# Performance work log

Measured on AMD Instinct MI355X. Metric: run time of the kernel, lower is better.

## Reference

```python
import jax, jax.numpy as jnp
import numpy as np

NEG_SLOPE = 0.01  # F.leaky_relu default


def gcn_conv(x, src, dst, norm, W, b, n_nodes):
    """PyG-style GCNConv: h = x @ W; out[i] = sum_{(j->i)} norm_e * h[j] + b.
    src/dst/norm already include self-loops and symmetric D^-1/2 A D^-1/2 weights."""
    h = x @ W                                   # [N, out]
    msgs = h[src] * norm[:, None]               # [E+N, out] gather
    out = jax.ops.segment_sum(msgs, dst, num_segments=n_nodes)  # scatter-add
    return out + b


def _build_norm(edge_idx, n_nodes):
    """Add self-loops and compute symmetric GCN normalization coefficients."""
    loops = jnp.arange(n_nodes, dtype=edge_idx.dtype)
    src = jnp.concatenate([edge_idx[0], loops])
    dst = jnp.concatenate([edge_idx[1], loops])
    deg = jax.ops.segment_sum(jnp.ones_like(dst, dtype=jnp.float32), dst,
                              num_segments=n_nodes)
    dinv = jnp.where(deg > 0, jax.lax.rsqrt(jnp.maximum(deg, 1.0)), 0.0)
    norm = dinv[src] * dinv[dst]
    return src, dst, norm


def setup_inputs() -> dict:
    key = jax.random.key(0)
    k = jax.random.split(key, 8)
    N, E, nfeat, nhid = 50000, 800000, 64, 64
    x = jax.random.normal(k[0], (N, nfeat), dtype=jnp.float32)
    edge_idx = jax.random.randint(k[1], (2, E), 0, N, dtype=jnp.int32)
    # inverted dropout mask, p=0.5 -> values in {0, 2}
    drop_mask = (jax.random.uniform(k[2], (N, nhid)) >= 0.5).astype(jnp.float32) * 2.0
    # glorot-style GCNConv weights + zero bias (PyG defaults)
    s1 = (6.0 / (nfeat + nhid)) ** 0.5
    s2 = (6.0 / (nhid + nhid // 2)) ** 0.5
    W1 = jax.random.uniform(k[3], (nfeat, nhid), minval=-s1, maxval=s1, dtype=jnp.float32)
    b1 = jnp.zeros((nhid,), dtype=jnp.float32)
    W2 = jax.random.uniform(k[4], (nhid, nhid // 2), minval=-s2, maxval=s2, dtype=jnp.float32)
    b2 = jnp.zeros((nhid // 2,), dtype=jnp.float32)
    return {"x": x, "edge_idx": edge_idx, "drop_mask": drop_mask,
            "W1": W1, "b1": b1, "W2": W2, "b2": b2}


def reference(x, edge_idx, drop_mask, W1, b1, W2, b2):
    n_nodes = x.shape[0]
    src, dst, norm = _build_norm(edge_idx, n_nodes)
    h = jax.nn.leaky_relu(gcn_conv(x, src, dst, norm, W1, b1, n_nodes), NEG_SLOPE)
    h = h * drop_mask  # F.dropout(p=0.5) with precomputed inverted mask
    out = jax.nn.leaky_relu(gcn_conv(h, src, dst, norm, W2, b2, n_nodes), NEG_SLOPE)
    return out
```

## Files before the change

kernel.cpp:

```cpp
#include <hip/hip_runtime.h>
#include <hip/hip_fp16.h>

#define NEG_SLOPE 0.01f
typedef unsigned int uint;
typedef unsigned short u16;

#define NBK 256
#define CHUNK 4096
#define KPT 16
#define GROWS 16

__device__ __forceinline__ void acc_row(uint2 v, float w,
                                        float& ax, float& ay, float& az, float& aw) {
    float2 f0 = __half22float2(*reinterpret_cast<__half2*>(&v.x));
    float2 f1 = __half22float2(*reinterpret_cast<__half2*>(&v.y));
    ax = fmaf(f0.x, w, ax); ay = fmaf(f0.y, w, ay);
    az = fmaf(f1.x, w, az); aw = fmaf(f1.y, w, aw);
}

__device__ __forceinline__ float wbits(uint rec) {
    u16 b = (u16)(rec >> 16);
    __half h;
    *reinterpret_cast<u16*>(&h) = b;
    return __half2float(h);
}

__global__ __launch_bounds__(256) void bucket_hist(const int* __restrict__ dst,
                                                   uint* __restrict__ hist,
                                                   int E) {
    __shared__ uint lh[NBK];
    int t = threadIdx.x;
    lh[t] = 0u;
    __syncthreads();
    int base = blockIdx.x * CHUNK;
#pragma unroll
    for (int r = 0; r < 4; ++r) {
        int e4 = base + r * 1024 + t * 4;
        if (e4 + 3 < E) {
            int4 d = *(const int4*)(dst + e4);
            atomicAdd(&lh[((uint)d.x) >> 8], 1u);
            atomicAdd(&lh[((uint)d.y) >> 8], 1u);
            atomicAdd(&lh[((uint)d.z) >> 8], 1u);
            atomicAdd(&lh[((uint)d.w) >> 8], 1u);
        } else {
            for (int e = e4; e < E && e < e4 + 4; ++e)
                atomicAdd(&lh[((uint)dst[e]) >> 8], 1u);
        }
    }
    __syncthreads();
    hist[(size_t)blockIdx.x * NBK + t] = lh[t];
}

__global__ __launch_bounds__(256) void scan_hist(uint* __restrict__ hist,
                                                 uint* __restrict__ buckTotal,
                                                 int nchunks) {
    __shared__ uint lds[256];
    int b = blockIdx.x;
    int t = threadIdx.x;
    uint carry = 0;
    for (int c0 = 0; c0 < nchunks; c0 += 256) {
        int c = c0 + t;
        uint v = (c < nchunks) ? hist[(size_t)c * NBK + b] : 0u;
        lds[t] = v;
        __syncthreads();
        for (int off = 1; off < 256; off <<= 1) {
            uint u = (t >= off) ? lds[t - off] : 0u;
            __syncthreads();
            lds[t] += u;
            __syncthreads();
        }
        uint incl = lds[t];
        if (c < nchunks) hist[(size_t)c * NBK + b] = carry + incl - v;
        uint tot = lds[255];
        __syncthreads();
        carry += tot;
    }
    if (t == 0) buckTotal[b] = carry;
}

__global__ __launch_bounds__(256) void scan256(const uint* __restrict__ buckTotal,
                                               uint* __restrict__ buckBase,
                                               int nbuck, int E) {
    __shared__ uint lds[256];
    int t = threadIdx.x;
    uint v = buckTotal[t];
    lds[t] = v;
    __syncthreads();
    for (int off = 1; off < 256; off <<= 1) {
        uint u = (t >= off) ? lds[t - off] : 0u;
        __syncthreads();
        lds[t] += u;
        __syncthreads();
    }
    buckBase[t] = (t < nbuck) ? (lds[t] - v) : (uint)E;
    if (t == 0) buckBase[NBK] = (uint)E;
}

__global__ __launch_bounds__(256) void partition_edges(const int* __restrict__ src,
                                                       const int* __restrict__ dst,
                                                       const uint* __restrict__ hist,
                                                       const uint* __restrict__ buckBase,
                                                       uint* __restrict__ staging,
                                                       int E) {
    __shared__ uint lh[NBK];
    __shared__ uint runbase[NBK];
    int t = threadIdx.x;
    lh[t] = 0u;
    __syncthreads();
    int base = blockIdx.x * CHUNK;
    uint rec[KPT], rb[KPT], rk[KPT];
#pragma unroll
    for (int r = 0; r < 4; ++r) {
        int e4 = base + r * 1024 + t * 4;
        if (e4 + 3 < E) {
            int4 s = *(const int4*)(src + e4);
            int4 d = *(const int4*)(dst + e4);
            int k = r * 4;
            rb[k + 0] = ((uint)d.x) >> 8; rec[k + 0] = (uint)s.x | (((uint)d.x & 255u) << 16);
            rb[k + 1] = ((uint)d.y) >> 8; rec[k + 1] = (uint)s.y | (((uint)d.y & 255u) << 16);
            rb[k + 2] = ((uint)d.z) >> 8; rec[k + 2] = (uint)s.z | (((uint)d.z & 255u) << 16);
            rb[k + 3] = ((uint)d.w) >> 8; rec[k + 3] = (uint)s.w | (((uint)d.w & 255u) << 16);
            rk[k + 0] = atomicAdd(&lh[rb[k + 0]], 1u);
            rk[k + 1] = atomicAdd(&lh[rb[k + 1]], 1u);
            rk[k + 2] = atomicAdd(&lh[rb[k + 2]], 1u);
            rk[k + 3] = atomicAdd(&lh[rb[k + 3]], 1u);
        } else {
            for (int j = 0; j < 4; ++j) {
                int e = e4 + j;
                int k = r * 4 + j;
                if (e < E) {
                    uint s = (uint)src[e], d = (uint)dst[e];
                    rb[k] = d >> 8;
                    rec[k] = s | ((d & 255u) << 16);
                    rk[k] = atomicAdd(&lh[rb[k]], 1u);
                } else rb[k] = 0xFFFFFFFFu;
            }
        }
    }
    __syncthreads();
    runbase[t] = buckBase[t] + hist[(size_t)blockIdx.x * NBK + t];
    __syncthreads();
#pragma unroll
    for (int k = 0; k < KPT; ++k)
        if (rb[k] != 0xFFFFFFFFu)
            staging[runbase[rb[k]] + rk[k]] = rec[k];
}

__global__ __launch_bounds__(256) void build_csr(const uint* __restrict__ staging,
                                                 const uint* __restrict__ buckBase,
                                                 u16* __restrict__ srcIdx,
                                                 uint* __restrict__ offs,
                                                 float* __restrict__ dinv,
                                                 int N, int nbuck) {
    __shared__ uint nh[256];
    __shared__ uint nstart[256];
    __shared__ u16 rankbuf[8192];
    __shared__ u16 outbuf[8192];
    int b = blockIdx.x;
    int t = threadIdx.x;
    uint base = buckBase[b], endb = buckBase[b + 1];
    uint T = endb - base;
    nh[t] = 0u;
    __syncthreads();
    for (uint i = t; i < T; i += 256) {
        uint rec = staging[base + i];
        rankbuf[i] = (u16)atomicAdd(&nh[(rec >> 16) & 255u], 1u);
    }
    __syncthreads();
    uint deg = nh[t];
    nstart[t] = deg;
    __syncthreads();
    for (int off = 1; off < 256; off <<= 1) {
        uint u = (t >= off) ? nstart[t - off] : 0u;
        __syncthreads();
        nstart[t] += u;
        __syncthreads();
    }
    uint excl = nstart[t] - deg;
    __syncthreads();
    nstart[t] = excl;
    __syncthreads();
    for (uint i = t; i < T; i += 256) {
        uint rec = staging[base + i];
        outbuf[nstart[(rec >> 16) & 255u] + rankbuf[i]] = (u16)(rec & 0xFFFFu);
    }
    __syncthreads();
    for (uint i = t; i < T; i += 256) srcIdx[base + i] = outbuf[i];
    int node = b * 256 + t;
    if (node < N) {
        offs[node] = base + excl;
        dinv[node] = rsqrtf((float)(deg + 1u));
    }
    if (b == nbuck - 1 && t == 0) offs[N] = endb;
}

__global__ __launch_bounds__(256) void fill_pack(const u16* __restrict__ srcIdx,
                                                 const float* __restrict__ dinv,
                                                 uint* __restrict__ packed, int E) {
    int i4 = (blockIdx.x * 256 + threadIdx.x) * 4;
    if (i4 + 3 < E) {
        ushort4 s = *(const ushort4*)(srcIdx + i4);
        uint4 o;
        __half h0 = __float2half(dinv[s.x]);
        __half h1 = __float2half(dinv[s.y]);
        __half h2 = __float2half(dinv[s.z]);
        __half h3 = __float2half(dinv[s.w]);
        o.x = (uint)s.x | ((uint)*reinterpret_cast<u16*>(&h0) << 16);
        o.y = (uint)s.y | ((uint)*reinterpret_cast<u16*>(&h1) << 16);
        o.z = (uint)s.z | ((uint)*reinterpret_cast<u16*>(&h2) << 16);
        o.w = (uint)s.w | ((uint)*reinterpret_cast<u16*>(&h3) << 16);
        *(uint4*)(packed + i4) = o;
    } else {
        for (int i = i4; i < E; ++i) {
            __half h = __float2half(dinv[srcIdx[i]]);
            packed[i] = (uint)srcIdx[i] | ((uint)*reinterpret_cast<u16*>(&h) << 16);
        }
    }
}

__global__ __launch_bounds__(256) void gemm64x64(const float* __restrict__ X,
                                                 const float* __restrict__ W,
                                                 __half* __restrict__ H, int N) {
    int lane = threadIdx.x & 63;
    int wv = threadIdx.x >> 6;
    float wc[64];
#pragma unroll
    for (int k = 0; k < 64; ++k) wc[k] = W[k * 64 + lane];
    int rowBase = (blockIdx.x * 4 + wv) * GROWS;
    for (int g = 0; g < GROWS; g += 4) {
        int r0 = __builtin_amdgcn_readfirstlane(rowBase + g);
        if (r0 >= N) return;
        int e1 = min(r0 + 1, N - 1), e2 = min(r0 + 2, N - 1), e3 = min(r0 + 3, N - 1);
        const float* x0 = X + (size_t)r0 * 64;
        const float* x1 = X + (size_t)e1 * 64;
        const float* x2 = X + (size_t)e2 * 64;
        const float* x3 = X + (size_t)e3 * 64;
        float a0 = 0.f, a1 = 0.f, a2 = 0.f, a3 = 0.f;
        float b0 = 0.f, b1 = 0.f, b2 = 0.f, b3 = 0.f;
#pragma unroll
        for (int k = 0; k < 64; k += 2) {
            a0 = fmaf(x0[k], wc[k], a0); b0 = fmaf(x0[k + 1], wc[k + 1], b0);
            a1 = fmaf(x1[k], wc[k], a1); b1 = fmaf(x1[k + 1], wc[k + 1], b1);
            a2 = fmaf(x2[k], wc[k], a2); b2 = fmaf(x2[k + 1], wc[k + 1], b2);
            a3 = fmaf(x3[k], wc[k], a3); b3 = fmaf(x3[k + 1], wc[k + 1], b3);
        }
        H[(size_t)r0 * 64 + lane] = __float2half(a0 + b0);
        if (r0 + 1 < N) H[(size_t)(r0 + 1) * 64 + lane] = __float2half(a1 + b1);
        if (r0 + 2 < N) H[(size_t)(r0 + 2) * 64 + lane] = __float2half(a2 + b2);
        if (r0 + 3 < N) H[(size_t)(r0 + 3) * 64 + lane] = __float2half(a3 + b3);
    }
}

__global__ __launch_bounds__(256) void gemm64x32(const float* __restrict__ X,
                                                 const float* __restrict__ W,
                                                 __half* __restrict__ H, int N) {
    int lane = threadIdx.x & 63;
    int col = lane & 31;
    int wv = threadIdx.x >> 6;
    float wc[64];
#pragma unroll
    for (int k = 0; k < 64; ++k) wc[k] = W[k * 32 + col];
    int rowBase = (blockIdx.x * 4 + wv) * GROWS;
    for (int g = 0; g < GROWS; g += 4) {
        int r0 = __builtin_amdgcn_readfirstlane(rowBase + g);
        if (r0 >= N) return;
        int e1 = min(r0 + 1, N - 1), e2 = min(r0 + 2, N - 1), e3 = min(r0 + 3, N - 1);
        const float* x0 = X + (size_t)r0 * 64;
        const float* x1 = X + (size_t)e1 * 64;
        const float* x2 = X + (size_t)e2 * 64;
        const float* x3 = X + (size_t)e3 * 64;
        float a0 = 0.f, a1 = 0.f, a2 = 0.f, a3 = 0.f;
        float b0 = 0.f, b1 = 0.f, b2 = 0.f, b3 = 0.f;
#pragma unroll
        for (int k = 0; k < 64; k += 2) {
            a0 = fmaf(x0[k], wc[k], a0); b0 = fmaf(x0[k + 1], wc[k + 1], b0);
            a1 = fmaf(x1[k], wc[k], a1); b1 = fmaf(x1[k + 1], wc[k + 1], b1);
            a2 = fmaf(x2[k], wc[k], a2); b2 = fmaf(x2[k + 1], wc[k + 1], b2);
            a3 = fmaf(x3[k], wc[k], a3); b3 = fmaf(x3[k + 1], wc[k + 1], b3);
        }
        if (lane < 32) {
            H[(size_t)r0 * 32 + col] = __float2half(a0 + b0);
            if (r0 + 1 < N) H[(size_t)(r0 + 1) * 32 + col] = __float2half(a1 + b1);
            if (r0 + 2 < N) H[(size_t)(r0 + 2) * 32 + col] = __float2half(a2 + b2);
            if (r0 + 3 < N) H[(size_t)(r0 + 3) * 32 + col] = __float2half(a3 + b3);
        }
    }
}

__global__ __launch_bounds__(256) void agg1(const __half* __restrict__ h,
                                            const uint* __restrict__ offs,
                                            const uint* __restrict__ packed,
                                            const float* __restrict__ dinv,
                                            const float* __restrict__ b,
                                            const float* __restrict__ mask,
                                            float* __restrict__ outp, int N) {
    int node = blockIdx.x * 4 + (threadIdx.x >> 6);
    if (node >= N) return;
    int lane = threadIdx.x & 63;
    int r = lane >> 4;
    int q = lane & 15;
    const uint2* h8 = (const uint2*)h;
    uint beg = offs[node], end = offs[node + 1];
    float ax = 0.f, ay = 0.f, az = 0.f, aw = 0.f;
    uint p = beg + (uint)r;
    for (; p + 12 < end; p += 16) {
        uint e0 = packed[p], e1 = packed[p + 4], e2 = packed[p + 8], e3 = packed[p + 12];
        float w0 = wbits(e0), w1 = wbits(e1), w2 = wbits(e2), w3 = wbits(e3);
        uint2 v0 = h8[(size_t)(e0 & 0xFFFFu) * 16 + q];
        uint2 v1 = h8[(size_t)(e1 & 0xFFFFu) * 16 + q];
        uint2 v2 = h8[(size_t)(e2 & 0xFFFFu) * 16 + q];
        uint2 v3 = h8[(size_t)(e3 & 0xFFFFu) * 16 + q];
        acc_row(v0, w0, ax, ay, az, aw);
        acc_row(v1, w1, ax, ay, az, aw);
        acc_row(v2, w2, ax, ay, az, aw);
        acc_row(v3, w3, ax, ay, az, aw);
    }
    for (; p < end; p += 4) {
        uint e0 = packed[p];
        float w0 = wbits(e0);
        uint2 v0 = h8[(size_t)(e0 & 0xFFFFu) * 16 + q];
        acc_row(v0, w0, ax, ay, az, aw);
    }
    ax += __shfl_xor(ax, 16, 64); ay += __shfl_xor(ay, 16, 64);
    az += __shfl_xor(az, 16, 64); aw += __shfl_xor(aw, 16, 64);
    ax += __shfl_xor(ax, 32, 64); ay += __shfl_xor(ay, 32, 64);
    az += __shfl_xor(az, 32, 64); aw += __shfl_xor(aw, 32, 64);
    if (r == 0) {
        float dv = dinv[node];
        float dv2 = dv * dv;
        uint2 hvv = h8[(size_t)node * 16 + q];
        float2 f0 = __half22float2(*reinterpret_cast<__half2*>(&hvv.x));
        float2 f1 = __half22float2(*reinterpret_cast<__half2*>(&hvv.y));
        float4 bv = ((const float4*)b)[q];
        float4 mv = ((const float4*)mask)[(size_t)node * 16 + q];
        float vx = ax * dv + f0.x * dv2 + bv.x;
        float vy = ay * dv + f0.y * dv2 + bv.y;
        float vz = az * dv + f1.x * dv2 + bv.z;
        float vw = aw * dv + f1.y * dv2 + bv.w;
        vx = (vx > 0.f) ? vx : NEG_SLOPE * vx;
        vy = (vy > 0.f) ? vy : NEG_SLOPE * vy;
        vz = (vz > 0.f) ? vz : NEG_SLOPE * vz;
        vw = (vw > 0.f) ? vw : NEG_SLOPE * vw;
        float4 o;
        o.x = vx * mv.x; o.y = vy * mv.y; o.z = vz * mv.z; o.w = vw * mv.w;
        ((float4*)outp)[(size_t)node * 16 + q] = o;
    }
}

__global__ __launch_bounds__(256) void agg2(const __half* __restrict__ h,
                                            const uint* __restrict__ offs,
                                            const uint* __restrict__ packed,
                                            const float* __restrict__ dinv,
                                            const float* __restrict__ b,
                                            float* __restrict__ outp, int N) {
    int node = blockIdx.x * 4 + (threadIdx.x >> 6);
    if (node >= N) return;
    int lane = threadIdx.x & 63;
    int r = lane >> 3;
    int q = lane & 7;
    const uint2* h8 = (const uint2*)h;
    uint beg = offs[node], end = offs[node + 1];
    float ax = 0.f, ay = 0.f, az = 0.f, aw = 0.f;
    uint p = beg + (uint)r;
    for (; p + 24 < end; p += 32) {
        uint e0 = packed[p], e1 = packed[p + 8], e2 = packed[p + 16], e3 = packed[p + 24];
        float w0 = wbits(e0), w1 = wbits(e1), w2 = wbits(e2), w3 = wbits(e3);
        uint2 v0 = h8[(size_t)(e0 & 0xFFFFu) * 8 + q];
        uint2 v1 = h8[(size_t)(e1 & 0xFFFFu) * 8 + q];
        uint2 v2 = h8[(size_t)(e2 & 0xFFFFu) * 8 + q];
        uint2 v3 = h8[(size_t)(e3 & 0xFFFFu) * 8 + q];
        acc_row(v0, w0, ax, ay, az, aw);
        acc_row(v1, w1, ax, ay, az, aw);
        acc_row(v2, w2, ax, ay, az, aw);
        acc_row(v3, w3, ax, ay, az, aw);
    }
    for (; p < end; p += 8) {
        uint e0 = packed[p];
        float w0 = wbits(e0);
        uint2 v0 = h8[(size_t)(e0 & 0xFFFFu) * 8 + q];
        acc_row(v0, w0, ax, ay, az, aw);
    }
    ax += __shfl_xor(ax, 8, 64);  ay += __shfl_xor(ay, 8, 64);
    az += __shfl_xor(az, 8, 64);  aw += __shfl_xor(aw, 8, 64);
    ax += __shfl_xor(ax, 16, 64); ay += __shfl_xor(ay, 16, 64);
    az += __shfl_xor(az, 16, 64); aw += __shfl_xor(aw, 16, 64);
    ax += __shfl_xor(ax, 32, 64); ay += __shfl_xor(ay, 32, 64);
    az += __shfl_xor(az, 32, 64); aw += __shfl_xor(aw, 32, 64);
    if (r == 0) {
        float dv = dinv[node];
        float dv2 = dv * dv;
        uint2 hvv = h8[(size_t)node * 8 + q];
        float2 f0 = __half22float2(*reinterpret_cast<__half2*>(&hvv.x));
        float2 f1 = __half22float2(*reinterpret_cast<__half2*>(&hvv.y));
        float4 bv = ((const float4*)b)[q];
        float vx = ax * dv + f0.x * dv2 + bv.x;
        float vy = ay * dv + f0.y * dv2 + bv.y;
        float vz = az * dv + f1.x * dv2 + bv.z;
        float vw = aw * dv + f1.y * dv2 + bv.w;
        float4 o;
        o.x = (vx > 0.f) ? vx : NEG_SLOPE * vx;
        o.y = (vy > 0.f) ? vy : NEG_SLOPE * vy;
        o.z = (vz > 0.f) ? vz : NEG_SLOPE * vz;
        o.w = (vw > 0.f) ? vw : NEG_SLOPE * vw;
        ((float4*)outp)[(size_t)node * 8 + q] = o;
    }
}

extern "C" void kernel_launch(void* const* d_in, const int* in_sizes, int n_in,
                              void* d_out, int out_size, void* d_ws, size_t ws_size,
                              hipStream_t stream) {
    const float* x    = (const float*)d_in[0];
    const int*   ei   = (const int*)d_in[1];
    const float* mask = (const float*)d_in[2];
    const float* W1   = (const float*)d_in[3];
    const float* b1   = (const float*)d_in[4];
    const float* W2   = (const float*)d_in[5];
    const float* b2   = (const float*)d_in[6];
    float* out = (float*)d_out;

    const int N = in_sizes[0] / 64;
    const int E = in_sizes[1] / 2;
    const int* src = ei;
    const int* dst = ei + E;

    const int nbuck  = (N + 255) >> 8;
    const int chunks = (E + CHUNK - 1) / CHUNK;
    const int gblocks = (N + 4 * GROWS - 1) / (4 * GROWS);

    char* w = (char*)d_ws;
    uint*  hist      = (uint*)w;    w += (size_t)chunks * NBK * 4;
    uint*  buckTotal = (uint*)w;    w += NBK * 4;
    uint*  buckBase  = (uint*)w;    w += (NBK + 1) * 4;
    w = (char*)(((size_t)w + 15) & ~15ull);
    uint*  offs      = (uint*)w;    w += (size_t)(N + 1) * 4;
    w = (char*)(((size_t)w + 15) & ~15ull);
    float* dinv      = (float*)w;   w += (size_t)N * 4;
    uint*  staging   = (uint*)w;    w += (size_t)E * 4;
    u16*   srcIdx    = (u16*)w;     w += (((size_t)E * 2 + 15) & ~15ull);
    uint*  packed    = (uint*)w;    w += (size_t)E * 4;
    __half* h1       = (__half*)w;  w += (size_t)N * 64 * 2;
    float* hpost     = (float*)w;   w += (size_t)N * 64 * 4;
    __half* h2       = h1;

    bucket_hist<<<chunks, 256, 0, stream>>>(dst, hist, E);
    scan_hist<<<NBK, 256, 0, stream>>>(hist, buckTotal, chunks);
    scan256<<<1, 256, 0, stream>>>(buckTotal, buckBase, nbuck, E);
    partition_edges<<<chunks, 256, 0, stream>>>(src, dst, hist, buckBase, staging, E);
    build_csr<<<nbuck, 256, 0, stream>>>(staging, buckBase, srcIdx, offs, dinv, N, nbuck);
    fill_pack<<<(E + 1023) / 1024, 256, 0, stream>>>(srcIdx, dinv, packed, E);

    gemm64x64<<<gblocks, 256, 0, stream>>>(x, W1, h1, N);
    agg1<<<(N + 3) / 4, 256, 0, stream>>>(h1, offs, packed, dinv, b1, mask, hpost, N);

    gemm64x32<<<gblocks, 256, 0, stream>>>(hpost, W2, h2, N);
    agg2<<<(N + 3) / 4, 256, 0, stream>>>(h2, offs, packed, dinv, b2, out, N);
}
```

Before: 136.0 us.

## Fold bucket scan into consumers, store hpost as fp16, widen agg gathers

Drops the single-block scan256 launch; partition_edges and build_csr now each redo the 256-entry bucket prefix scan in LDS. The agg1 output (hpost) is stored as fp16 instead of fp32 and gemm64x32 reads fp16, halving that intermediate's traffic. Both aggregation kernels switch to 16-byte uint4 gathers with 8 accumulators per lane and adjusted lane/edge splits. The cost is a redundant scan in every block and extra fp16 rounding of the dropout-masked hidden activations.

```diff
diff --git a/kernel.cpp b/kernel.cpp
--- a/kernel.cpp
+++ b/kernel.cpp
@@ -9,20 +9,28 @@
 #define CHUNK 4096
 #define KPT 16
 #define GROWS 16
-
-__device__ __forceinline__ void acc_row(uint2 v, float w,
-                                        float& ax, float& ay, float& az, float& aw) {
-    float2 f0 = __half22float2(*reinterpret_cast<__half2*>(&v.x));
-    float2 f1 = __half22float2(*reinterpret_cast<__half2*>(&v.y));
-    ax = fmaf(f0.x, w, ax); ay = fmaf(f0.y, w, ay);
-    az = fmaf(f1.x, w, az); aw = fmaf(f1.y, w, aw);
-}
 
 __device__ __forceinline__ float wbits(uint rec) {
     u16 b = (u16)(rec >> 16);
     __half h;
     *reinterpret_cast<u16*>(&h) = b;
     return __half2float(h);
+}
+
+__device__ __forceinline__ void acc8(uint4 v, float w, float* a) {
+    float2 f;
+    f = __half22float2(*reinterpret_cast<__half2*>(&v.x)); a[0] = fmaf(f.x, w, a[0]); a[1] = fmaf(f.y, w, a[1]);
+    f = __half22float2(*reinterpret_cast<__half2*>(&v.y)); a[2] = fmaf(f.x, w, a[2]); a[3] = fmaf(f.y, w, a[3]);
+    f = __half22float2(*reinterpret_cast<__half2*>(&v.z)); a[4] = fmaf(f.x, w, a[4]); a[5] = fmaf(f.y, w, a[5]);
+    f = __half22float2(*reinterpret_cast<__half2*>(&v.w)); a[6] = fmaf(f.x, w, a[6]); a[7] = fmaf(f.y, w, a[7]);
+}
+
+__device__ __forceinline__ void unpack8(uint4 v, float* s) {
+    float2 f;
+    f = __half22float2(*reinterpret_cast<__half2*>(&v.x)); s[0] = f.x; s[1] = f.y;
+    f = __half22float2(*reinterpret_cast<__half2*>(&v.y)); s[2] = f.x; s[3] = f.y;
+    f = __half22float2(*reinterpret_cast<__half2*>(&v.z)); s[4] = f.x; s[5] = f.y;
+    f = __half22float2(*reinterpret_cast<__half2*>(&v.w)); s[6] = f.x; s[7] = f.y;
 }
 
 __global__ __launch_bounds__(256) void bucket_hist(const int* __restrict__ dst,
@@ -78,35 +86,26 @@
     if (t == 0) buckTotal[b] = carry;
 }
 
-__global__ __launch_bounds__(256) void scan256(const uint* __restrict__ buckTotal,
-                                               uint* __restrict__ buckBase,
-                                               int nbuck, int E) {
-    __shared__ uint lds[256];
-    int t = threadIdx.x;
-    uint v = buckTotal[t];
-    lds[t] = v;
-    __syncthreads();
-    for (int off = 1; off < 256; off <<= 1) {
-        uint u = (t >= off) ? lds[t - off] : 0u;
-        __syncthreads();
-        lds[t] += u;
-        __syncthreads();
-    }
-    buckBase[t] = (t < nbuck) ? (lds[t] - v) : (uint)E;
-    if (t == 0) buckBase[NBK] = (uint)E;
-}
-
 __global__ __launch_bounds__(256) void partition_edges(const int* __restrict__ src,
                                                        const int* __restrict__ dst,
                                                        const uint* __restrict__ hist,
-                                                       const uint* __restrict__ buckBase,
+                                                       const uint* __restrict__ buckTotal,
                                                        uint* __restrict__ staging,
                                                        int E) {
     __shared__ uint lh[NBK];
+    __shared__ uint sc[NBK];
     __shared__ uint runbase[NBK];
     int t = threadIdx.x;
     lh[t] = 0u;
-    __syncthreads();
+    uint tot = buckTotal[t];
+    sc[t] = tot;
+    __syncthreads();
+    for (int off = 1; off < NBK; off <<= 1) {
+        uint u = (t >= off) ? sc[t - off] : 0u;
+        __syncthreads();
+        sc[t] += u;
+        __syncthreads();
+    }
     int base = blockIdx.x * CHUNK;
     uint rec[KPT], rb[KPT], rk[KPT];
 #pragma unroll
@@ -138,7 +137,7 @@
         }
     }
     __syncthreads();
-    runbase[t] = buckBase[t] + hist[(size_t)blockIdx.x * NBK + t];
+    runbase[t] = (sc[t] - tot) + hist[(size_t)blockIdx.x * NBK + t];
     __syncthreads();
 #pragma unroll
     for (int k = 0; k < KPT; ++k)
@@ -147,7 +146,7 @@
 }
 
 __global__ __launch_bounds__(256) void build_csr(const uint* __restrict__ staging,
-                                                 const uint* __restrict__ buckBase,
+                                                 const uint* __restrict__ buckTotal,
                                                  u16* __restrict__ srcIdx,
                                                  uint* __restrict__ offs,
                                                  float* __restrict__ dinv,
@@ -158,7 +157,18 @@
     __shared__ u16 outbuf[8192];
     int b = blockIdx.x;
     int t = threadIdx.x;
-    uint base = buckBase[b], endb = buckBase[b + 1];
+    uint tot = buckTotal[t];
+    nstart[t] = tot;
+    __syncthreads();
+    for (int off = 1; off < NBK; off <<= 1) {
+        uint u = (t >= off) ? nstart[t - off] : 0u;
+        __syncthreads();
+        nstart[t] += u;
+        __syncthreads();
+    }
+    uint endb = nstart[b];
+    uint base = endb - buckTotal[b];
+    __syncthreads();
     uint T = endb - base;
     nh[t] = 0u;
     __syncthreads();
@@ -251,7 +261,7 @@
     }
 }
 
-__global__ __launch_bounds__(256) void gemm64x32(const float* __restrict__ X,
+__global__ __launch_bounds__(256) void gemm64x32(const __half* __restrict__ Xh,
                                                  const float* __restrict__ W,
                                                  __half* __restrict__ H, int N) {
     int lane = threadIdx.x & 63;
@@ -265,18 +275,23 @@
         int r0 = __builtin_amdgcn_readfirstlane(rowBase + g);
         if (r0 >= N) return;
         int e1 = min(r0 + 1, N - 1), e2 = min(r0 + 2, N - 1), e3 = min(r0 + 3, N - 1);
-        const float* x0 = X + (size_t)r0 * 64;
-        const float* x1 = X + (size_t)e1 * 64;
-        const float* x2 = X + (size_t)e2 * 64;
-        const float* x3 = X + (size_t)e3 * 64;
+        const uint* x0 = (const uint*)(Xh + (size_t)r0 * 64);
+        const uint* x1 = (const uint*)(Xh + (size_t)e1 * 64);
+        const uint* x2 = (const uint*)(Xh + (size_t)e2 * 64);
+        const uint* x3 = (const uint*)(Xh + (size_t)e3 * 64);
         float a0 = 0.f, a1 = 0.f, a2 = 0.f, a3 = 0.f;
         float b0 = 0.f, b1 = 0.f, b2 = 0.f, b3 = 0.f;
 #pragma unroll
-        for (int k = 0; k < 64; k += 2) {
-            a0 = fmaf(x0[k], wc[k], a0); b0 = fmaf(x0[k + 1], wc[k + 1], b0);
-            a1 = fmaf(x1[k], wc[k], a1); b1 = fmaf(x1[k + 1], wc[k + 1], b1);
-            a2 = fmaf(x2[k], wc[k], a2); b2 = fmaf(x2[k + 1], wc[k + 1], b2);
-            a3 = fmaf(x3[k], wc[k], a3); b3 = fmaf(x3[k + 1], wc[k + 1], b3);
+        for (int kk = 0; kk < 32; ++kk) {
+            uint u0 = x0[kk], u1 = x1[kk], u2 = x2[kk], u3 = x3[kk];
+            float2 f0 = __half22float2(*reinterpret_cast<__half2*>(&u0));
+            float2 f1 = __half22float2(*reinterpret_cast<__half2*>(&u1));
+            float2 f2 = __half22float2(*reinterpret_cast<__half2*>(&u2));
+            float2 f3 = __half22float2(*reinterpret_cast<__half2*>(&u3));
+            a0 = fmaf(f0.x, wc[2 * kk], a0); b0 = fmaf(f0.y, wc[2 * kk + 1], b0);
+            a1 = fmaf(f1.x, wc[2 * kk], a1); b1 = fmaf(f1.y, wc[2 * kk + 1], b1);
+            a2 = fmaf(f2.x, wc[2 * kk], a2); b2 = fmaf(f2.y, wc[2 * kk + 1], b2);
+            a3 = fmaf(f3.x, wc[2 * kk], a3); b3 = fmaf(f3.y, wc[2 * kk + 1], b3);
         }
         if (lane < 32) {
             H[(size_t)r0 * 32 + col] = __float2half(a0 + b0);
@@ -293,57 +308,62 @@
                                             const float* __restrict__ dinv,
                                             const float* __restrict__ b,
                                             const float* __restrict__ mask,
-                                            float* __restrict__ outp, int N) {
+                                            __half* __restrict__ outp, int N) {
     int node = blockIdx.x * 4 + (threadIdx.x >> 6);
     if (node >= N) return;
     int lane = threadIdx.x & 63;
-    int r = lane >> 4;
-    int q = lane & 15;
-    const uint2* h8 = (const uint2*)h;
+    int r = lane >> 3;
+    int q = lane & 7;
+    const uint4* h16 = (const uint4*)h;
     uint beg = offs[node], end = offs[node + 1];
-    float ax = 0.f, ay = 0.f, az = 0.f, aw = 0.f;
+    float a[8] = {0.f, 0.f, 0.f, 0.f, 0.f, 0.f, 0.f, 0.f};
     uint p = beg + (uint)r;
-    for (; p + 12 < end; p += 16) {
-        uint e0 = packed[p], e1 = packed[p + 4], e2 = packed[p + 8], e3 = packed[p + 12];
-        float w0 = wbits(e0), w1 = wbits(e1), w2 = wbits(e2), w3 = wbits(e3);
-        uint2 v0 = h8[(size_t)(e0 & 0xFFFFu) * 16 + q];
-        uint2 v1 = h8[(size_t)(e1 & 0xFFFFu) * 16 + q];
-        uint2 v2 = h8[(size_t)(e2 & 0xFFFFu) * 16 + q];
-        uint2 v3 = h8[(size_t)(e3 & 0xFFFFu) * 16 + q];
-        acc_row(v0, w0, ax, ay, az, aw);
-        acc_row(v1, w1, ax, ay, az, aw);
-        acc_row(v2, w2, ax, ay, az, aw);
-        acc_row(v3, w3, ax, ay, az, aw);
-    }
-    for (; p < end; p += 4) {
+    for (; p + 24 < end; p += 32) {
+        uint e0 = packed[p], e1 = packed[p + 8], e2 = packed[p + 16], e3 = packed[p + 24];
+        uint4 v0 = h16[(size_t)(e0 & 0xFFFFu) * 8 + q];
+        uint4 v1 = h16[(size_t)(e1 & 0xFFFFu) * 8 + q];
+        uint4 v2 = h16[(size_t)(e2 & 0xFFFFu) * 8 + q];
+        uint4 v3 = h16[(size_t)(e3 & 0xFFFFu) * 8 + q];
+        acc8(v0, wbits(e0), a);
+        acc8(v1, wbits(e1), a);
+        acc8(v2, wbits(e2), a);
+        acc8(v3, wbits(e3), a);
+    }
+    for (; p < end; p += 8) {
         uint e0 = packed[p];
-        float w0 = wbits(e0);
-        uint2 v0 = h8[(size_t)(e0 & 0xFFFFu) * 16 + q];
-        acc_row(v0, w0, ax, ay, az, aw);
-    }
-    ax += __shfl_xor(ax, 16, 64); ay += __shfl_xor(ay, 16, 64);
-    az += __shfl_xor(az, 16, 64); aw += __shfl_xor(aw, 16, 64);
-    ax += __shfl_xor(ax, 32, 64); ay += __shfl_xor(ay, 32, 64);
-    az += __shfl_xor(az, 32, 64); aw += __shfl_xor(aw, 32, 64);
+        uint4 v0 = h16[(size_t)(e0 & 0xFFFFu) * 8 + q];
+        acc8(v0, wbits(e0), a);
+    }
+#pragma unroll
+    for (int i = 0; i < 8; ++i) {
+        a[i] += __shfl_xor(a[i], 8, 64);
+        a[i] += __shfl_xor(a[i], 16, 64);
+        a[i] += __shfl_xor(a[i], 32, 64);
+    }
     if (r == 0) {
         float dv = dinv[node];
         float dv2 = dv * dv;
-        uint2 hvv = h8[(size_t)node * 16 + q];
-        float2 f0 = __half22float2(*reinterpret_cast<__half2*>(&hvv.x));
-        float2 f1 = __half22float2(*reinterpret_cast<__half2*>(&hvv.y));
-        float4 bv = ((const float4*)b)[q];
-        float4 mv = ((const float4*)mask)[(size_t)node * 16 + q];
-        float vx = ax * dv + f0.x * dv2 + bv.x;
-        float vy = ay * dv + f0.y * dv2 + bv.y;
-        float vz = az * dv + f1.x * dv2 + bv.z;
-        float vw = aw * dv + f1.y * dv2 + bv.w;
-        vx = (vx > 0.f) ? vx : NEG_SLOPE * vx;
-        vy = (vy > 0.f) ? vy : NEG_SLOPE * vy;
-        vz = (vz > 0.f) ? vz : NEG_SLOPE * vz;
-        vw = (vw > 0.f) ? vw : NEG_SLOPE * vw;
-        float4 o;
-        o.x = vx * mv.x; o.y = vy * mv.y; o.z = vz * mv.z; o.w = vw * mv.w;
-        ((float4*)outp)[(size_t)node * 16 + q] = o;
+        float s[8];
+        unpack8(h16[(size_t)node * 8 + q], s);
+        float4 bv0 = ((const float4*)b)[q * 2];
+        float4 bv1 = ((const float4*)b)[q * 2 + 1];
+        float4 mv0 = ((const float4*)mask)[(size_t)node * 16 + q * 2];
+        float4 mv1 = ((const float4*)mask)[(size_t)node * 16 + q * 2 + 1];
+        float bb[8] = {bv0.x, bv0.y, bv0.z, bv0.w, bv1.x, bv1.y, bv1.z, bv1.w};
+        float mm[8] = {mv0.x, mv0.y, mv0.z, mv0.w, mv1.x, mv1.y, mv1.z, mv1.w};
+        uint4 o;
+        uint* op = (uint*)&o;
+#pragma unroll
+        for (int i = 0; i < 4; ++i) {
+            float v0 = a[2 * i] * dv + s[2 * i] * dv2 + bb[2 * i];
+            float v1 = a[2 * i + 1] * dv + s[2 * i + 1] * dv2 + bb[2 * i + 1];
+            v0 = (v0 > 0.f) ? v0 : NEG_SLOPE * v0;
+            v1 = (v1 > 0.f) ? v1 : NEG_SLOPE * v1;
+            v0 *= mm[2 * i]; v1 *= mm[2 * i + 1];
+            __half2 hh = __floats2half2_rn(v0, v1);
+            op[i] = *reinterpret_cast<uint*>(&hh);
+        }
+        ((uint4*)outp)[(size_t)node * 8 + q] = o;
     }
 }
 
@@ -356,53 +376,48 @@
     int node = blockIdx.x * 4 + (threadIdx.x >> 6);
     if (node >= N) return;
     int lane = threadIdx.x & 63;
-    int r = lane >> 3;
-    int q = lane & 7;
-    const uint2* h8 = (const uint2*)h;
+    int r = lane >> 2;
+    int q = lane & 3;
+    const uint4* h8 = (const uint4*)h;
     uint beg = offs[node], end = offs[node + 1];
-    float ax = 0.f, ay = 0.f, az = 0.f, aw = 0.f;
+    float a[8] = {0.f, 0.f, 0.f, 0.f, 0.f, 0.f, 0.f, 0.f};
     uint p = beg + (uint)r;
-    for (; p + 24 < end; p += 32) {
-        uint e0 = packed[p], e1 = packed[p + 8], e2 = packed[p + 16], e3 = packed[p + 24];
-        float w0 = wbits(e0), w1 = wbits(e1), w2 = wbits(e2), w3 = wbits(e3);
-        uint2 v0 = h8[(size_t)(e0 & 0xFFFFu) * 8 + q];
-        uint2 v1 = h8[(size_t)(e1 & 0xFFFFu) * 8 + q];
-        uint2 v2 = h8[(size_t)(e2 & 0xFFFFu) * 8 + q];
-        uint2 v3 = h8[(size_t)(e3 & 0xFFFFu) * 8 + q];
-        acc_row(v0, w0, ax, ay, az, aw);
-        acc_row(v1, w1, ax, ay, az, aw);
-        acc_row(v2, w2, ax, ay, az, aw);
-        acc_row(v3, w3, ax, ay, az, aw);
-    }
-    for (; p < end; p += 8) {
+    for (; p + 16 < end; p += 32) {
+        uint e0 = packed[p], e1 = packed[p + 16];
+        uint4 v0 = h8[(size_t)(e0 & 0xFFFFu) * 4 + q];
+        uint4 v1 = h8[(size_t)(e1 & 0xFFFFu) * 4 + q];
+        acc8(v0, wbits(e0), a);
+        acc8(v1, wbits(e1), a);
+    }
+    for (; p < end; p += 16) {
         uint e0 = packed[p];
-        float w0 = wbits(e0);
-        uint2 v0 = h8[(size_t)(e0 & 0xFFFFu) * 8 + q];
-        acc_row(v0, w0, ax, ay, az, aw);
-    }
-    ax += __shfl_xor(ax, 8, 64);  ay += __shfl_xor(ay, 8, 64);
-    az += __shfl_xor(az, 8, 64);  aw += __shfl_xor(aw, 8, 64);
-    ax += __shfl_xor(ax, 16, 64); ay += __shfl_xor(ay, 16, 64);
-    az += __shfl_xor(az, 16, 64); aw += __shfl_xor(aw, 16, 64);
-    ax += __shfl_xor(ax, 32, 64); ay += __shfl_xor(ay, 32, 64);
-    az += __shfl_xor(az, 32, 64); aw += __shfl_xor(aw, 32, 64);
+        uint4 v0 = h8[(size_t)(e0 & 0xFFFFu) * 4 + q];
+        acc8(v0, wbits(e0), a);
+    }
+#pragma unroll
+    for (int i = 0; i < 8; ++i) {
+        a[i] += __shfl_xor(a[i], 4, 64);
+        a[i] += __shfl_xor(a[i], 8, 64);
+        a[i] += __shfl_xor(a[i], 16, 64);
+        a[i] += __shfl_xor(a[i], 32, 64);
+    }
     if (r == 0) {
         float dv = dinv[node];
         float dv2 = dv * dv;
-        uint2 hvv = h8[(size_t)node * 8 + q];
-        float2 f0 = __half22float2(*reinterpret_cast<__half2*>(&hvv.x));
-        float2 f1 = __half22float2(*reinterpret_cast<__half2*>(&hvv.y));
-        float4 bv = ((const float4*)b)[q];
-        float vx = ax * dv + f0.x * dv2 + bv.x;
-        float vy = ay * dv + f0.y * dv2 + bv.y;
-        float vz = az * dv + f1.x * dv2 + bv.z;
-        float vw = aw * dv + f1.y * dv2 + bv.w;
-        float4 o;
-        o.x = (vx > 0.f) ? vx : NEG_SLOPE * vx;
-        o.y = (vy > 0.f) ? vy : NEG_SLOPE * vy;
-        o.z = (vz > 0.f) ? vz : NEG_SLOPE * vz;
-        o.w = (vw > 0.f) ? vw : NEG_SLOPE * vw;
-        ((float4*)outp)[(size_t)node * 8 + q] = o;
+        float s[8];
+        unpack8(h8[(size_t)node * 4 + q], s);
+        float4 bv0 = ((const float4*)b)[q * 2];
+        float4 bv1 = ((const float4*)b)[q * 2 + 1];
+        float bb[8] = {bv0.x, bv0.y, bv0.z, bv0.w, bv1.x, bv1.y, bv1.z, bv1.w};
+        float o[8];
+#pragma unroll
+        for (int i = 0; i < 8; ++i) {
+            float v = a[i] * dv + s[i] * dv2 + bb[i];
+            o[i] = (v > 0.f) ? v : NEG_SLOPE * v;
+        }
+        float4* outv = (float4*)outp;
+        outv[(size_t)node * 8 + q * 2]     = make_float4(o[0], o[1], o[2], o[3]);
+        outv[(size_t)node * 8 + q * 2 + 1] = make_float4(o[4], o[5], o[6], o[7]);
     }
 }
 
@@ -430,7 +445,6 @@
     char* w = (char*)d_ws;
     uint*  hist      = (uint*)w;    w += (size_t)chunks * NBK * 4;
     uint*  buckTotal = (uint*)w;    w += NBK * 4;
-    uint*  buckBase  = (uint*)w;    w += (NBK + 1) * 4;
     w = (char*)(((size_t)w + 15) & ~15ull);
     uint*  offs      = (uint*)w;    w += (size_t)(N + 1) * 4;
     w = (char*)(((size_t)w + 15) & ~15ull);
@@ -439,14 +453,13 @@
     u16*   srcIdx    = (u16*)w;     w += (((size_t)E * 2 + 15) & ~15ull);
     uint*  packed    = (uint*)w;    w += (size_t)E * 4;
     __half* h1       = (__half*)w;  w += (size_t)N * 64 * 2;
-    float* hpost     = (float*)w;   w += (size_t)N * 64 * 4;
+    __half* hpost    = (__half*)w;  w += (size_t)N * 64 * 2;
     __half* h2       = h1;
 
     bucket_hist<<<chunks, 256, 0, stream>>>(dst, hist, E);
     scan_hist<<<NBK, 256, 0, stream>>>(hist, buckTotal, chunks);
-    scan256<<<1, 256, 0, stream>>>(buckTotal, buckBase, nbuck, E);
-    partition_edges<<<chunks, 256, 0, stream>>>(src, dst, hist, buckBase, staging, E);
-    build_csr<<<nbuck, 256, 0, stream>>>(staging, buckBase, srcIdx, offs, dinv, N, nbuck);
+    partition_edges<<<chunks, 256, 0, stream>>>(src, dst, hist, buckTotal, staging, E);
+    build_csr<<<nbuck, 256, 0, stream>>>(staging, buckTotal, srcIdx, offs, dinv, N, nbuck);
     fill_pack<<<(E + 1023) / 1024, 256, 0, stream>>>(srcIdx, dinv, packed, E);
 
     gemm64x64<<<gblocks, 256, 0, stream>>>(x, W1, h1, N);
```

New measurement: 129.6 us. 4.7% less time.
